# Performance work log

Measured on AMD Instinct MI355X. Metric: run time of the kernel, lower is better.

The kernel has to match this reference:

```python
import jax, jax.numpy as jnp
import numpy as np

B, S, H = 2, 2048, 2048
NQ, NKV = 32, 8
HD = H // NQ  # 64


def setup_inputs() -> dict:
    key = jax.random.key(0)
    ks = jax.random.split(key, 9)
    s = 1.0 / np.sqrt(H)
    return {
        "x": jax.random.normal(ks[0], (B, S, H), dtype=jnp.float32),
        "Wq": jax.random.normal(ks[1], (H, H), dtype=jnp.float32) * s,
        "bq": jnp.zeros((H,), dtype=jnp.float32),
        "Wk": jax.random.normal(ks[2], (H, NKV * HD), dtype=jnp.float32) * s,
        "bk": jnp.zeros((NKV * HD,), dtype=jnp.float32),
        "Wv": jax.random.normal(ks[3], (H, NKV * HD), dtype=jnp.float32) * s,
        "bv": jnp.zeros((NKV * HD,), dtype=jnp.float32),
        "Wo": jax.random.normal(ks[4], (H, H), dtype=jnp.float32) * s,
        "bo": jnp.zeros((H,), dtype=jnp.float32),
    }


def reference(x, Wq, bq, Wk, bk, Wv, bv, Wo, bo):
    Bx, Sx, _ = x.shape
    g = NQ // NKV  # queries per kv head
    q = (x @ Wq + bq).reshape(Bx, Sx, NKV, g, HD)   # grouped query heads
    k = (x @ Wk + bk).reshape(Bx, Sx, NKV, HD)
    v = (x @ Wv + bv).reshape(Bx, Sx, NKV, HD)
    # scores: [B, NKV, g, S, S] -- broadcast KV across group instead of jnp.repeat
    scores = jnp.einsum('bshgd,bkhd->bhgsk', q, k) / jnp.sqrt(jnp.float32(HD))
    probs = jax.nn.softmax(scores, axis=-1)
    out = jnp.einsum('bhgsk,bkhd->bshgd', probs, v).reshape(Bx, Sx, H)
    return out @ Wo + bo
```

## Files before the change

### kernel.cpp

```cpp
#include <hip/hip_runtime.h>
#include <cstdint>
#include <cstddef>

typedef unsigned short u16;
typedef __bf16 bf16x8 __attribute__((ext_vector_type(8)));
typedef float f32x4 __attribute__((ext_vector_type(4)));
typedef unsigned short u16x4 __attribute__((ext_vector_type(4)));
typedef unsigned short u16x8 __attribute__((ext_vector_type(8)));
typedef uint32_t u32x4 __attribute__((ext_vector_type(4)));
typedef __attribute__((address_space(1))) unsigned int as1_uint;
typedef __attribute__((address_space(3))) unsigned int as3_uint;

__device__ __forceinline__ u16 f2bf(float f) {
  uint32_t u = __builtin_bit_cast(uint32_t, f);
  u += 0x7FFFu + ((u >> 16) & 1u);
  return (u16)(u >> 16);
}

__device__ __forceinline__ uint32_t cvtpk2bf(float a, float b) {
  uint32_t r;
  asm("v_cvt_pk_bf16_f32 %0, %1, %2" : "=v"(r) : "v"(a), "v"(b));
  return r;
}

__device__ __forceinline__ float max3f(float a, float b, float c) {
  return fmaxf(fmaxf(a, b), c);
}

__device__ __forceinline__ void gld_lds16(const void* g, void* l) {
  __builtin_amdgcn_global_load_lds((as1_uint*)g, (as3_uint*)l, 16, 0, 0);
}

__global__ __launch_bounds__(256) void k_cast(const float* __restrict__ in,
                                              u16* __restrict__ out, int n8) {
  int i = blockIdx.x * 256 + threadIdx.x;
  if (i >= n8) return;
  const float4* p = reinterpret_cast<const float4*>(in) + (size_t)i * 2;
  float4 a = p[0], b = p[1];
  u16x8 r;
  r[0] = f2bf(a.x); r[1] = f2bf(a.y); r[2] = f2bf(a.z); r[3] = f2bf(a.w);
  r[4] = f2bf(b.x); r[5] = f2bf(b.y); r[6] = f2bf(b.z); r[7] = f2bf(b.w);
  *reinterpret_cast<u16x8*>(out + (size_t)i * 8) = r;
}

__global__ __launch_bounds__(256) void k_transpose_cast(const float* __restrict__ W,
                                                        u16* __restrict__ Wt,
                                                        int K, int N) {
  __shared__ u16 tile[64][72];
  int k0 = blockIdx.y * 64, n0 = blockIdx.x * 64;
  int r = threadIdx.x >> 4;
  int c4 = (threadIdx.x & 15) * 4;
#pragma unroll
  for (int i = 0; i < 4; ++i) {
    int kk = r + i * 16;
    float4 v = *reinterpret_cast<const float4*>(W + (size_t)(k0 + kk) * N + n0 + c4);
    tile[kk][c4 + 0] = f2bf(v.x); tile[kk][c4 + 1] = f2bf(v.y);
    tile[kk][c4 + 2] = f2bf(v.z); tile[kk][c4 + 3] = f2bf(v.w);
  }
  __syncthreads();
#pragma unroll
  for (int i = 0; i < 4; ++i) {
    int nn = r + i * 16;
    u16x4 o;
    o[0] = tile[c4 + 0][nn]; o[1] = tile[c4 + 1][nn];
    o[2] = tile[c4 + 2][nn]; o[3] = tile[c4 + 3][nn];
    *reinterpret_cast<u16x4*>(Wt + (size_t)(n0 + nn) * K + k0 + c4) = o;
  }
}

__global__ __launch_bounds__(256) void k_concat_bias(const float* __restrict__ bq,
                                                     const float* __restrict__ bk,
                                                     const float* __restrict__ bv,
                                                     float* __restrict__ out) {
  int i = blockIdx.x * 256 + threadIdx.x;
  if (i >= 3072) return;
  float v;
  if (i < 2048) v = bq[i];
  else if (i < 2560) v = bk[i - 2048];
  else v = bv[i - 2560];
  out[i] = v;
}

template <bool F32OUT>
__global__ __launch_bounds__(256) void k_gemm(const u16* __restrict__ A,
                                              const u16* __restrict__ Bt,
                                              const float* __restrict__ bias,
                                              void* __restrict__ Cout,
                                              int M, int N, int K,
                                              int scaleN, float scaleV) {
  __shared__ __align__(16) u16 As[128 * 64];
  __shared__ __align__(16) u16 Bs[128 * 64];
  const int m0 = blockIdx.y * 128, n0 = blockIdx.x * 128;
  const int tid = threadIdx.x;
  const int l = tid & 63, w = tid >> 6;
  const int wm = w >> 1, wn = w & 1;
  const int lr = l & 15, lo = l >> 4;
  const int srow = w * 8 + (l >> 3);
  const int sc = (l & 7) ^ ((l >> 3) & 7);
  f32x4 acc[4][4] = {};
  for (int kt = 0; kt < K; kt += 64) {
    __syncthreads();
#pragma unroll
    for (int it = 0; it < 4; ++it) {
      int row = it * 32 + srow;
      gld_lds16(A + (size_t)(m0 + row) * K + kt + sc * 8,
                (char*)As + (it * 32 + w * 8) * 128);
      gld_lds16(Bt + (size_t)(n0 + row) * K + kt + sc * 8,
                (char*)Bs + (it * 32 + w * 8) * 128);
    }
    __syncthreads();
    bf16x8 af[4][2], bfr[4][2];
#pragma unroll
    for (int mi = 0; mi < 4; ++mi) {
      int row = wm * 64 + mi * 16 + lr;
#pragma unroll
      for (int ks = 0; ks < 2; ++ks) {
        int ch = (ks * 4 + lo) ^ (row & 7);
        af[mi][ks] = *reinterpret_cast<const bf16x8*>((const char*)As + row * 128 + ch * 16);
      }
    }
#pragma unroll
    for (int nj = 0; nj < 4; ++nj) {
      int row = wn * 64 + nj * 16 + lr;
#pragma unroll
      for (int ks = 0; ks < 2; ++ks) {
        int ch = (ks * 4 + lo) ^ (row & 7);
        bfr[nj][ks] = *reinterpret_cast<const bf16x8*>((const char*)Bs + row * 128 + ch * 16);
      }
    }
#pragma unroll
    for (int mi = 0; mi < 4; ++mi)
#pragma unroll
      for (int nj = 0; nj < 4; ++nj) {
        acc[mi][nj] = __builtin_amdgcn_mfma_f32_16x16x32_bf16(af[mi][0], bfr[nj][0], acc[mi][nj], 0, 0, 0);
        acc[mi][nj] = __builtin_amdgcn_mfma_f32_16x16x32_bf16(af[mi][1], bfr[nj][1], acc[mi][nj], 0, 0, 0);
      }
  }
#pragma unroll
  for (int mi = 0; mi < 4; ++mi) {
    int row = m0 + wm * 64 + mi * 16 + lo * 4;
#pragma unroll
    for (int nj = 0; nj < 4; ++nj) {
      int col = n0 + wn * 64 + nj * 16 + lr;
      float bv = bias[col];
      float scc = (col < scaleN) ? scaleV : 1.0f;
#pragma unroll
      for (int r = 0; r < 4; ++r) {
        float v = (acc[mi][nj][r] + bv) * scc;
        if (F32OUT) ((float*)Cout)[(size_t)(row + r) * N + col] = v;
        else        ((u16*)Cout)[(size_t)(row + r) * N + col] = f2bf(v);
      }
    }
  }
}

__global__ __launch_bounds__(256, 4) void k_attn(const u16* __restrict__ QKV,
                                                 u16* __restrict__ Oa) {
  constexpr int S = 2048, LDQ = 3072, LDV = 72;
  constexpr float THR = 8.0f;
  __shared__ __align__(16) u16 Ks[2][64 * 64];
  __shared__ __align__(16) u16 Vt[2][64 * LDV];
  const int qt = blockIdx.x, h = blockIdx.y, b = blockIdx.z;
  const int kvh = h >> 2;
  const int tid = threadIdx.x, l = tid & 63, w = tid >> 6;
  const int lr = l & 15, lo = l >> 4;
  const size_t base = (size_t)b * S * LDQ;
  const u16* Qg = QKV + base + h * 64;
  const u16* Kg = QKV + base + 2048 + kvh * 64;
  const u16* Vg = QKV + base + 2560 + kvh * 64;
  const int qrow = qt * 64 + w * 16 + lr;
  const bf16x8 aq0 = *reinterpret_cast<const bf16x8*>(Qg + (size_t)qrow * LDQ + lo * 8);
  const bf16x8 aq1 = *reinterpret_cast<const bf16x8*>(Qg + (size_t)qrow * LDQ + 32 + lo * 8);
  f32x4 acc[4] = {};
  float mrun = -1e30f, lsum = 0.f;
  const int krow = w * 8 + (l >> 3);
  const int ksc = (l & 7) ^ ((l >> 3) & 7);
  const int vkey = (l & 31) * 2;
  const int vdh = (l >> 5) * 8;
  gld_lds16(Kg + (size_t)(krow) * LDQ + ksc * 8, (char*)Ks[0] + (w * 8) * 128);
  gld_lds16(Kg + (size_t)(32 + krow) * LDQ + ksc * 8, (char*)Ks[0] + (32 + w * 8) * 128);
  u16x8 va = *reinterpret_cast<const u16x8*>(Vg + (size_t)(vkey) * LDQ + w * 16 + vdh);
  u16x8 vb = *reinterpret_cast<const u16x8*>(Vg + (size_t)(vkey + 1) * LDQ + w * 16 + vdh);
  int cur = 0;
  for (int kt = 0; kt < S; kt += 64) {
#pragma unroll
    for (int j = 0; j < 8; ++j) {
      uint32_t pw = (uint32_t)va[j] | ((uint32_t)vb[j] << 16);
      *reinterpret_cast<uint32_t*>(&Vt[cur][(w * 16 + vdh + j) * LDV + vkey]) = pw;
    }
    __syncthreads();
    if (kt + 64 < S) {
      gld_lds16(Kg + (size_t)(kt + 64 + krow) * LDQ + ksc * 8, (char*)Ks[cur ^ 1] + (w * 8) * 128);
      gld_lds16(Kg + (size_t)(kt + 96 + krow) * LDQ + ksc * 8, (char*)Ks[cur ^ 1] + (32 + w * 8) * 128);
      va = *reinterpret_cast<const u16x8*>(Vg + (size_t)(kt + 64 + vkey) * LDQ + w * 16 + vdh);
      vb = *reinterpret_cast<const u16x8*>(Vg + (size_t)(kt + 64 + vkey + 1) * LDQ + w * 16 + vdh);
    }
    float p[16];
    const u16* KsC = Ks[cur];
    __builtin_amdgcn_s_setprio(1);
#pragma unroll
    for (int t = 0; t < 4; ++t) {
      const int row = t * 16 + lr;
      bf16x8 k0 = *reinterpret_cast<const bf16x8*>((const char*)KsC + row * 128 + ((lo ^ (row & 7)) * 16));
      bf16x8 k1 = *reinterpret_cast<const bf16x8*>((const char*)KsC + row * 128 + (((4 + lo) ^ (row & 7)) * 16));
      f32x4 zz = {};
      zz = __builtin_amdgcn_mfma_f32_16x16x32_bf16(k0, aq0, zz, 0, 0, 0);
      zz = __builtin_amdgcn_mfma_f32_16x16x32_bf16(k1, aq1, zz, 0, 0, 0);
#pragma unroll
      for (int r = 0; r < 4; ++r) p[t * 4 + r] = zz[r];
    }
    __builtin_amdgcn_s_setprio(0);
    float m0 = max3f(p[0], p[1], p[2]);
    float m1 = max3f(p[3], p[4], p[5]);
    float m2 = max3f(p[6], p[7], p[8]);
    float m3 = max3f(p[9], p[10], p[11]);
    float m4 = max3f(p[12], p[13], p[14]);
    float tm = fmaxf(max3f(m0, m1, m2), max3f(m3, m4, p[15]));
    tm = fmaxf(tm, __shfl_xor(tm, 16, 64));
    tm = fmaxf(tm, __shfl_xor(tm, 32, 64));
    if (__all(tm <= mrun + THR)) {
#pragma unroll
      for (int i = 0; i < 16; ++i) p[i] = __builtin_amdgcn_exp2f(p[i] - mrun);
    } else {
      float mnew = fmaxf(mrun, tm);
      float alpha = __builtin_amdgcn_exp2f(mrun - mnew);
      mrun = mnew;
#pragma unroll
      for (int i = 0; i < 16; ++i) p[i] = __builtin_amdgcn_exp2f(p[i] - mnew);
      lsum *= alpha;
#pragma unroll
      for (int r = 0; r < 4; ++r) {
        float ar = __shfl(alpha, lo * 4 + r, 64);
#pragma unroll
        for (int nj = 0; nj < 4; ++nj) acc[nj][r] *= ar;
      }
    }
    float rs = (((p[0] + p[1]) + (p[2] + p[3])) + ((p[4] + p[5]) + (p[6] + p[7])))
             + (((p[8] + p[9]) + (p[10] + p[11])) + ((p[12] + p[13]) + (p[14] + p[15])));
    rs += __shfl_xor(rs, 16, 64);
    rs += __shfl_xor(rs, 32, 64);
    lsum += rs;
    uint32_t w00 = cvtpk2bf(p[0], p[1]),   w01 = cvtpk2bf(p[2], p[3]);
    uint32_t w10 = cvtpk2bf(p[4], p[5]),   w11 = cvtpk2bf(p[6], p[7]);
    uint32_t w20 = cvtpk2bf(p[8], p[9]),   w21 = cvtpk2bf(p[10], p[11]);
    uint32_t w30 = cvtpk2bf(p[12], p[13]), w31 = cvtpk2bf(p[14], p[15]);
    asm volatile("v_permlane32_swap_b32 %0, %1" : "+v"(w00), "+v"(w10));
    asm volatile("v_permlane16_swap_b32 %0, %1" : "+v"(w00), "+v"(w10));
    asm volatile("v_permlane32_swap_b32 %0, %1" : "+v"(w01), "+v"(w11));
    asm volatile("v_permlane16_swap_b32 %0, %1" : "+v"(w01), "+v"(w11));
    asm volatile("v_permlane32_swap_b32 %0, %1" : "+v"(w20), "+v"(w30));
    asm volatile("v_permlane16_swap_b32 %0, %1" : "+v"(w20), "+v"(w30));
    asm volatile("v_permlane32_swap_b32 %0, %1" : "+v"(w21), "+v"(w31));
    asm volatile("v_permlane16_swap_b32 %0, %1" : "+v"(w21), "+v"(w31));
    u32x4 pq0; pq0[0] = w00; pq0[1] = w01; pq0[2] = w10; pq0[3] = w11;
    u32x4 pq1; pq1[0] = w20; pq1[1] = w21; pq1[2] = w30; pq1[3] = w31;
    const bf16x8 pa0 = __builtin_bit_cast(bf16x8, pq0);
    const bf16x8 pa1 = __builtin_bit_cast(bf16x8, pq1);
    const u16* VtC = Vt[cur];
    __builtin_amdgcn_s_setprio(1);
#pragma unroll
    for (int nj = 0; nj < 4; ++nj) {
      const bf16x8 bv0 = *reinterpret_cast<const bf16x8*>(&VtC[(nj * 16 + lr) * LDV + lo * 8]);
      const bf16x8 bv1 = *reinterpret_cast<const bf16x8*>(&VtC[(nj * 16 + lr) * LDV + 32 + lo * 8]);
      acc[nj] = __builtin_amdgcn_mfma_f32_16x16x32_bf16(pa0, bv0, acc[nj], 0, 0, 0);
      acc[nj] = __builtin_amdgcn_mfma_f32_16x16x32_bf16(pa1, bv1, acc[nj], 0, 0, 0);
    }
    __builtin_amdgcn_s_setprio(0);
    cur ^= 1;
  }
  float lf[4];
#pragma unroll
  for (int r = 0; r < 4; ++r) lf[r] = 1.0f / __shfl(lsum, lo * 4 + r, 64);
  const size_t orow = (size_t)b * S + qt * 64 + w * 16 + lo * 4;
#pragma unroll
  for (int nj = 0; nj < 4; ++nj) {
    const int col = h * 64 + nj * 16 + lr;
#pragma unroll
    for (int r = 0; r < 4; ++r)
      Oa[(orow + r) * 2048 + col] = f2bf(acc[nj][r] * lf[r]);
  }
}

extern "C" void kernel_launch(void* const* d_in, const int* in_sizes, int n_in,
                              void* d_out, int out_size, void* d_ws, size_t ws_size,
                              hipStream_t stream) {
  const float* x  = (const float*)d_in[0];
  const float* Wq = (const float*)d_in[1];
  const float* bq = (const float*)d_in[2];
  const float* Wk = (const float*)d_in[3];
  const float* bk = (const float*)d_in[4];
  const float* Wv = (const float*)d_in[5];
  const float* bv = (const float*)d_in[6];
  const float* Wo = (const float*)d_in[7];
  const float* bo = (const float*)d_in[8];
  float* out = (float*)d_out;
  char* ws = (char*)d_ws;

  u16*   xb    = (u16*)(ws + 0);
  u16*   wqkvT = (u16*)(ws + 16777216);
  u16*   woT   = (u16*)(ws + 29360128);
  u16*   qkv   = (u16*)(ws + 37748736);
  u16*   attn  = (u16*)(ws + 62914560);
  float* bcat  = (float*)(ws + 79691776);

  const float SCL = 0.125f * 1.44269504088896341f;

  k_cast<<<4096, 256, 0, stream>>>(x, xb, 1048576);
  k_transpose_cast<<<dim3(32, 32), 256, 0, stream>>>(Wq, wqkvT, 2048, 2048);
  k_transpose_cast<<<dim3(8, 32), 256, 0, stream>>>(Wk, wqkvT + (size_t)2048 * 2048, 2048, 512);
  k_transpose_cast<<<dim3(8, 32), 256, 0, stream>>>(Wv, wqkvT + (size_t)2560 * 2048, 2048, 512);
  k_transpose_cast<<<dim3(32, 32), 256, 0, stream>>>(Wo, woT, 2048, 2048);
  k_concat_bias<<<12, 256, 0, stream>>>(bq, bk, bv, bcat);
  k_gemm<false><<<dim3(24, 32), 256, 0, stream>>>(xb, wqkvT, bcat, qkv, 4096, 3072, 2048, 2048, SCL);
  k_attn<<<dim3(32, 32, 2), 256, 0, stream>>>(qkv, attn);
  k_gemm<true><<<dim3(16, 32), 256, 0, stream>>>(attn, woT, bo, out, 4096, 2048, 2048, 0, 1.0f);
}
```

Before: 299.0 us.

## Pre-transpose V in a separate kernel and async-load it into LDS

Adds a kernel that transposes the V slice of the QKV buffer into a [b,kvh,d,seq] layout, reusing the x-cast workspace region. The attention kernel then loads V tiles with direct global-to-LDS copies and an XOR-swizzled layout, the same path K uses. This removes the per-iteration register pack and LDS scatter writes for V. The cost is an extra kernel launch and an extra round trip of V through global memory.

```diff
diff --git a/kernel.cpp b/kernel.cpp
--- a/kernel.cpp
+++ b/kernel.cpp
@@ -65,6 +65,32 @@
     o[0] = tile[c4 + 0][nn]; o[1] = tile[c4 + 1][nn];
     o[2] = tile[c4 + 2][nn]; o[3] = tile[c4 + 3][nn];
     *reinterpret_cast<u16x4*>(Wt + (size_t)(n0 + nn) * K + k0 + c4) = o;
+  }
+}
+
+__global__ __launch_bounds__(256) void k_transpose_v(const u16* __restrict__ qkv,
+                                                     u16* __restrict__ vt) {
+  __shared__ u16 tile[64][72];
+  const int t0 = blockIdx.x * 64, kvh = blockIdx.y, b = blockIdx.z;
+  const u16* src = qkv + ((size_t)(b * 2048) + t0) * 3072 + 2560 + kvh * 64;
+  u16* dst = vt + ((size_t)(b * 8 + kvh) * 64) * 2048 + t0;
+  const int r = threadIdx.x >> 3;
+  const int c8 = (threadIdx.x & 7) * 8;
+#pragma unroll
+  for (int i = 0; i < 2; ++i) {
+    int rr = r + i * 32;
+    u16x8 v = *reinterpret_cast<const u16x8*>(src + (size_t)rr * 3072 + c8);
+#pragma unroll
+    for (int j = 0; j < 8; ++j) tile[c8 + j][rr] = v[j];
+  }
+  __syncthreads();
+#pragma unroll
+  for (int i = 0; i < 2; ++i) {
+    int rr = r + i * 32;
+    u16x8 o;
+#pragma unroll
+    for (int j = 0; j < 8; ++j) o[j] = tile[rr][c8 + j];
+    *reinterpret_cast<u16x8*>(dst + (size_t)rr * 2048 + c8) = o;
   }
 }
 
@@ -155,11 +181,12 @@
 }
 
 __global__ __launch_bounds__(256, 4) void k_attn(const u16* __restrict__ QKV,
+                                                 const u16* __restrict__ VT,
                                                  u16* __restrict__ Oa) {
-  constexpr int S = 2048, LDQ = 3072, LDV = 72;
+  constexpr int S = 2048, LDQ = 3072;
   constexpr float THR = 8.0f;
   __shared__ __align__(16) u16 Ks[2][64 * 64];
-  __shared__ __align__(16) u16 Vt[2][64 * LDV];
+  __shared__ __align__(16) u16 Vs[2][64 * 64];
   const int qt = blockIdx.x, h = blockIdx.y, b = blockIdx.z;
   const int kvh = h >> 2;
   const int tid = threadIdx.x, l = tid & 63, w = tid >> 6;
@@ -167,7 +194,7 @@
   const size_t base = (size_t)b * S * LDQ;
   const u16* Qg = QKV + base + h * 64;
   const u16* Kg = QKV + base + 2048 + kvh * 64;
-  const u16* Vg = QKV + base + 2560 + kvh * 64;
+  const u16* Vg = VT + (size_t)(b * 8 + kvh) * 64 * 2048;
   const int qrow = qt * 64 + w * 16 + lr;
   const bf16x8 aq0 = *reinterpret_cast<const bf16x8*>(Qg + (size_t)qrow * LDQ + lo * 8);
   const bf16x8 aq1 = *reinterpret_cast<const bf16x8*>(Qg + (size_t)qrow * LDQ + 32 + lo * 8);
@@ -175,25 +202,19 @@
   float mrun = -1e30f, lsum = 0.f;
   const int krow = w * 8 + (l >> 3);
   const int ksc = (l & 7) ^ ((l >> 3) & 7);
-  const int vkey = (l & 31) * 2;
-  const int vdh = (l >> 5) * 8;
-  gld_lds16(Kg + (size_t)(krow) * LDQ + ksc * 8, (char*)Ks[0] + (w * 8) * 128);
+  gld_lds16(Kg + (size_t)krow * LDQ + ksc * 8, (char*)Ks[0] + (w * 8) * 128);
   gld_lds16(Kg + (size_t)(32 + krow) * LDQ + ksc * 8, (char*)Ks[0] + (32 + w * 8) * 128);
-  u16x8 va = *reinterpret_cast<const u16x8*>(Vg + (size_t)(vkey) * LDQ + w * 16 + vdh);
-  u16x8 vb = *reinterpret_cast<const u16x8*>(Vg + (size_t)(vkey + 1) * LDQ + w * 16 + vdh);
+  gld_lds16(Vg + (size_t)krow * 2048 + ksc * 8, (char*)Vs[0] + (w * 8) * 128);
+  gld_lds16(Vg + (size_t)(32 + krow) * 2048 + ksc * 8, (char*)Vs[0] + (32 + w * 8) * 128);
   int cur = 0;
   for (int kt = 0; kt < S; kt += 64) {
-#pragma unroll
-    for (int j = 0; j < 8; ++j) {
-      uint32_t pw = (uint32_t)va[j] | ((uint32_t)vb[j] << 16);
-      *reinterpret_cast<uint32_t*>(&Vt[cur][(w * 16 + vdh + j) * LDV + vkey]) = pw;
-    }
     __syncthreads();
     if (kt + 64 < S) {
-      gld_lds16(Kg + (size_t)(kt + 64 + krow) * LDQ + ksc * 8, (char*)Ks[cur ^ 1] + (w * 8) * 128);
-      gld_lds16(Kg + (size_t)(kt + 96 + krow) * LDQ + ksc * 8, (char*)Ks[cur ^ 1] + (32 + w * 8) * 128);
-      va = *reinterpret_cast<const u16x8*>(Vg + (size_t)(kt + 64 + vkey) * LDQ + w * 16 + vdh);
-      vb = *reinterpret_cast<const u16x8*>(Vg + (size_t)(kt + 64 + vkey + 1) * LDQ + w * 16 + vdh);
+      const int nb = cur ^ 1, nk = kt + 64;
+      gld_lds16(Kg + (size_t)(nk + krow) * LDQ + ksc * 8, (char*)Ks[nb] + (w * 8) * 128);
+      gld_lds16(Kg + (size_t)(nk + 32 + krow) * LDQ + ksc * 8, (char*)Ks[nb] + (32 + w * 8) * 128);
+      gld_lds16(Vg + (size_t)krow * 2048 + nk + ksc * 8, (char*)Vs[nb] + (w * 8) * 128);
+      gld_lds16(Vg + (size_t)(32 + krow) * 2048 + nk + ksc * 8, (char*)Vs[nb] + (32 + w * 8) * 128);
     }
     float p[16];
     const u16* KsC = Ks[cur];
@@ -256,12 +277,13 @@
     u32x4 pq1; pq1[0] = w20; pq1[1] = w21; pq1[2] = w30; pq1[3] = w31;
     const bf16x8 pa0 = __builtin_bit_cast(bf16x8, pq0);
     const bf16x8 pa1 = __builtin_bit_cast(bf16x8, pq1);
-    const u16* VtC = Vt[cur];
+    const u16* VsC = Vs[cur];
     __builtin_amdgcn_s_setprio(1);
 #pragma unroll
     for (int nj = 0; nj < 4; ++nj) {
-      const bf16x8 bv0 = *reinterpret_cast<const bf16x8*>(&VtC[(nj * 16 + lr) * LDV + lo * 8]);
-      const bf16x8 bv1 = *reinterpret_cast<const bf16x8*>(&VtC[(nj * 16 + lr) * LDV + 32 + lo * 8]);
+      const int vr = nj * 16 + lr;
+      const bf16x8 bv0 = *reinterpret_cast<const bf16x8*>((const char*)VsC + vr * 128 + ((lo ^ (vr & 7)) * 16));
+      const bf16x8 bv1 = *reinterpret_cast<const bf16x8*>((const char*)VsC + vr * 128 + (((4 + lo) ^ (vr & 7)) * 16));
       acc[nj] = __builtin_amdgcn_mfma_f32_16x16x32_bf16(pa0, bv0, acc[nj], 0, 0, 0);
       acc[nj] = __builtin_amdgcn_mfma_f32_16x16x32_bf16(pa1, bv1, acc[nj], 0, 0, 0);
     }
@@ -297,6 +319,7 @@
   char* ws = (char*)d_ws;
 
   u16*   xb    = (u16*)(ws + 0);
+  u16*   vtg   = (u16*)(ws + 0);
   u16*   wqkvT = (u16*)(ws + 16777216);
   u16*   woT   = (u16*)(ws + 29360128);
   u16*   qkv   = (u16*)(ws + 37748736);
@@ -312,6 +335,7 @@
   k_transpose_cast<<<dim3(32, 32), 256, 0, stream>>>(Wo, woT, 2048, 2048);
   k_concat_bias<<<12, 256, 0, stream>>>(bq, bk, bv, bcat);
   k_gemm<false><<<dim3(24, 32), 256, 0, stream>>>(xb, wqkvT, bcat, qkv, 4096, 3072, 2048, 2048, SCL);
-  k_attn<<<dim3(32, 32, 2), 256, 0, stream>>>(qkv, attn);
+  k_transpose_v<<<dim3(32, 8, 2), 256, 0, stream>>>(qkv, vtg);
+  k_attn<<<dim3(32, 32, 2), 256, 0, stream>>>(qkv, vtg, attn);
   k_gemm<true><<<dim3(16, 32), 256, 0, stream>>>(attn, woT, bo, out, 4096, 2048, 2048, 0, 1.0f);
 }
```

Measured after the change: 291.9 us. 2.4% less time.
